# Kernel optimization log

Hardware: AMD Instinct MI355X
Metric: run time of the kernel (lower is better)

The kernel has to match this reference:

```python
import jax, jax.numpy as jnp
import numpy as np

B, S, D = 2, 2048, 1024
H = 16
HD = D // H  # 64


def setup_inputs() -> dict:
    key = jax.random.key(0)
    k1, k2, k3, k4, k5, k6 = jax.random.split(key, 6)
    hidden_states = jax.random.normal(k1, (B, S, D), dtype=jnp.float32)
    attention_mask = jax.random.randint(k2, (B, S), 0, 2, dtype=jnp.int32)
    scale = 1.0 / np.sqrt(D)
    Wq = jax.random.normal(k3, (D, D), dtype=jnp.float32) * scale
    bq = jax.random.normal(k4, (D,), dtype=jnp.float32) * 0.02
    Wk = jax.random.normal(k5, (D, D), dtype=jnp.float32) * scale
    bk = jax.random.normal(k6, (D,), dtype=jnp.float32) * 0.02
    return {"hidden_states": hidden_states, "attention_mask": attention_mask,
            "Wq": Wq, "bq": bq, "Wk": Wk, "bk": bk}


def _split_heads(x):
    # [B, S, D] -> [B, H, S, HD]
    b, s, _ = x.shape
    return x.reshape(b, s, H, HD).transpose(0, 2, 1, 3)


def reference(hidden_states, attention_mask, Wq, bq, Wk, bk):
    dh = jnp.sqrt(jnp.float32(HD))
    q = _split_heads(hidden_states @ Wq + bq)            # [B,H,S,HD]
    k = _split_heads(hidden_states @ Wk + bk)            # [B,H,S,HD]
    v = q + k                                            # value = Q + K
    k_t = -jax.nn.log_sigmoid(-k)                        # negate the logsigmoid(-K) transform
    scores = jnp.einsum('bhqd,bhkd->bhqk', q, k_t) / dh  # [B,H,S,S]
    # mask applied on the QUERY axis (dim 2), broadcast over key axis (faithful to source)
    mask = (attention_mask[:, None, :, None] == 0)       # [B,1,S,1]
    scores = jnp.where(mask, jnp.float32(-10000.0), scores)
    probs = jax.nn.softmax(scores, axis=-1)              # dropout: eval mode (identity)
    ctx = jnp.einsum('bhqk,bhkd->bhqd', probs, v)        # [B,H,S,HD]
    ctx = ctx.transpose(0, 2, 1, 3).reshape(B, S, D)
    return ctx
```

## Files before the change

kernel.cpp:

```cpp
#include <hip/hip_runtime.h>
#include <hip/hip_bf16.h>

#define B_ 2
#define S_ 2048
#define D_ 1024
#define H_ 16
#define HD_ 64

typedef __attribute__((ext_vector_type(8))) short short8;
typedef __attribute__((ext_vector_type(4))) short short4v;
typedef __attribute__((ext_vector_type(4))) float float4v;

typedef const __attribute__((address_space(1))) void* gas_ptr;
typedef __attribute__((address_space(3))) void* las_ptr;

static __device__ inline void gl_lds16(const void* g, void* l) {
  __builtin_amdgcn_global_load_lds((gas_ptr)g, (las_ptr)l, 16, 0, 0);
}

static __device__ inline float b2f(__hip_bfloat16 h) { return __bfloat162float(h); }

static __device__ inline short f2bs(float x) {
  __hip_bfloat16 h = __float2bfloat16(x);
  union { __hip_bfloat16 h; short s; } u; u.h = h; return u.s;
}
static __device__ inline float bs2f(short s) {
  union { short s; __hip_bfloat16 h; } u; u.s = s; return __bfloat162float(u.h);
}
static __device__ inline short4v pk4(float a, float b, float c, float d) {
  union { __hip_bfloat162 h[2]; short4v s; } u;
  u.h[0] = __float22bfloat162_rn(float2{a, b});
  u.h[1] = __float22bfloat162_rn(float2{c, d});
  return u.s;
}

static __device__ inline float4v mfma32(short8 a, short8 b, float4v c) {
  return __builtin_amdgcn_mfma_f32_16x16x32_bf16(a, b, c, 0, 0, 0);
}
static __device__ inline float4v mfma16(short4v a, short4v b, float4v c) {
  return __builtin_amdgcn_mfma_f32_16x16x16bf16_1k(a, b, c, 0, 0, 0);
}

__global__ __launch_bounds__(256) void pre(
    const float* __restrict__ Wq, const float* __restrict__ Wk,
    const float* __restrict__ hs,
    __hip_bfloat16* __restrict__ Wqt, __hip_bfloat16* __restrict__ Wkt,
    __hip_bfloat16* __restrict__ hsb) {
  if (blockIdx.z == 2) {
    const int blk = blockIdx.y * 16 + blockIdx.x;
    for (int it = 0; it < 8; ++it) {
      const size_t i = (size_t)blk * 16384 + it * 2048 + threadIdx.x * 8;
      const float4v v0 = *(const float4v*)(hs + i);
      const float4v v1 = *(const float4v*)(hs + i + 4);
      short8 s;
      for (int j = 0; j < 4; ++j) { s[j] = f2bs(v0[j]); s[4 + j] = f2bs(v1[j]); }
      *(short8*)(hsb + i) = s;
    }
    return;
  }
  const float* W = blockIdx.z ? Wk : Wq;
  __hip_bfloat16* Wt = blockIdx.z ? Wkt : Wqt;
  __shared__ float t[64][65];
  const int n0 = blockIdx.x * 64, k0 = blockIdx.y * 64;
  const int c = threadIdx.x & 63, r0 = threadIdx.x >> 6;
  for (int i = 0; i < 16; ++i) {
    const int r = i * 4 + r0;
    t[c][r] = W[(size_t)(k0 + r) * D_ + n0 + c];
  }
  __syncthreads();
  for (int i = 0; i < 16; ++i) {
    const int rr = i * 4 + r0;
    Wt[(size_t)(n0 + rr) * D_ + k0 + c] = __float2bfloat16(t[rr][c]);
  }
}

__global__ __launch_bounds__(256) void gemm_fused(
    const __hip_bfloat16* __restrict__ A,
    const __hip_bfloat16* __restrict__ Wqt, const __hip_bfloat16* __restrict__ Wkt,
    const float* __restrict__ bq, const float* __restrict__ bk,
    __hip_bfloat16* __restrict__ q_out, __hip_bfloat16* __restrict__ kt_out,
    __hip_bfloat16* __restrict__ vT) {
  const int n0 = blockIdx.x * 128, m0 = blockIdx.y * 64;
  __shared__ __hip_bfloat16 As[2][64 * 32];
  __shared__ __hip_bfloat16 Bq[2][128 * 32];
  __shared__ __hip_bfloat16 Bk[2][128 * 32];
  const int tid = threadIdx.x, wid = tid >> 6, lane = tid & 63;
  const int wm = (wid >> 1) * 32, wn = (wid & 1) * 64;
  const int l15 = lane & 15, l4 = lane >> 4;
  const float4v zz = {0.f, 0.f, 0.f, 0.f};
  float4v accq[2][4], acck[2][4];
  for (int i = 0; i < 2; ++i)
    for (int j = 0; j < 4; ++j) { accq[i][j] = zz; acck[i][j] = zz; }
  const int arow = wid * 16 + (lane >> 2);
  const int brow = wid * 32 + (lane >> 2);
  const int lk8 = (lane & 3) * 8;
  gl_lds16(A + (size_t)(m0 + arow) * D_ + lk8, As[0] + wid * 512);
  gl_lds16(Wqt + (size_t)(n0 + brow) * D_ + lk8, Bq[0] + wid * 1024);
  gl_lds16(Wqt + (size_t)(n0 + brow + 16) * D_ + lk8, Bq[0] + wid * 1024 + 512);
  gl_lds16(Wkt + (size_t)(n0 + brow) * D_ + lk8, Bk[0] + wid * 1024);
  gl_lds16(Wkt + (size_t)(n0 + brow + 16) * D_ + lk8, Bk[0] + wid * 1024 + 512);
  int p = 0;
  for (int kb = 0; kb < 32; ++kb) {
    __syncthreads();
    if (kb < 31) {
      const int kc = (kb + 1) * 32 + lk8;
      gl_lds16(A + (size_t)(m0 + arow) * D_ + kc, As[p ^ 1] + wid * 512);
      gl_lds16(Wqt + (size_t)(n0 + brow) * D_ + kc, Bq[p ^ 1] + wid * 1024);
      gl_lds16(Wqt + (size_t)(n0 + brow + 16) * D_ + kc, Bq[p ^ 1] + wid * 1024 + 512);
      gl_lds16(Wkt + (size_t)(n0 + brow) * D_ + kc, Bk[p ^ 1] + wid * 1024);
      gl_lds16(Wkt + (size_t)(n0 + brow + 16) * D_ + kc, Bk[p ^ 1] + wid * 1024 + 512);
    }
    short8 af[2], bfq[4], bfk[4];
    const int fo = l4 * 8;
    for (int rt = 0; rt < 2; ++rt)
      af[rt] = *(const short8*)(As[p] + (wm + rt * 16 + l15) * 32 + fo);
    for (int ct = 0; ct < 4; ++ct) {
      bfq[ct] = *(const short8*)(Bq[p] + (wn + ct * 16 + l15) * 32 + fo);
      bfk[ct] = *(const short8*)(Bk[p] + (wn + ct * 16 + l15) * 32 + fo);
    }
    for (int rt = 0; rt < 2; ++rt)
      for (int ct = 0; ct < 4; ++ct) {
        accq[rt][ct] = mfma32(af[rt], bfq[ct], accq[rt][ct]);
        acck[rt][ct] = mfma32(af[rt], bfk[ct], acck[rt][ct]);
      }
    p ^= 1;
  }
  float bvq[4], bvk[4];
  for (int ct = 0; ct < 4; ++ct) {
    bvq[ct] = bq[n0 + wn + ct * 16 + l15];
    bvk[ct] = bk[n0 + wn + ct * 16 + l15];
  }
  for (int rt = 0; rt < 2; ++rt)
    for (int ct = 0; ct < 4; ++ct) {
      const int col = n0 + wn + ct * 16 + l15;
      const int h = col >> 6, d = col & 63;
      const int rowb = m0 + wm + rt * 16 + l4 * 4;
      short4v vv;
      for (int r = 0; r < 4; ++r) {
        const int row = rowb + r;
        const float qv = accq[rt][ct][r] + bvq[ct];
        const float kv = acck[rt][ct][r] + bvk[ct];
        const float sp = fmaxf(kv, 0.f) + __logf(1.f + __expf(-fabsf(kv)));
        q_out[(size_t)row * D_ + col] = __float2bfloat16(qv);
        kt_out[(size_t)row * D_ + col] = __float2bfloat16(sp);
        vv[r] = f2bs(qv + kv);
      }
      const int b = rowb >> 11, s = rowb & 2047;
      *(short4v*)(vT + ((size_t)(b * H_ + h) * HD_ + d) * S_ + s) = vv;
    }
}

__global__ __launch_bounds__(256, 4) void attn(
    const __hip_bfloat16* __restrict__ qb, const __hip_bfloat16* __restrict__ ktb,
    const __hip_bfloat16* __restrict__ vT, const int* __restrict__ mask,
    float* __restrict__ out) {
  __shared__ short smem[17664];
  const int q0 = blockIdx.x * 128, h = blockIdx.y, b = blockIdx.z;
  const int tid = threadIdx.x, wid = tid >> 6, lane = tid & 63;
  const int l15 = lane & 15, l4 = lane >> 4;
  const __hip_bfloat16* qh = qb + (size_t)b * S_ * D_ + h * HD_;
  const __hip_bfloat16* kh = ktb + (size_t)b * S_ * D_ + h * HD_;
  const __hip_bfloat16* vh = vT + (size_t)(b * H_ + h) * HD_ * S_;
  const int srow = tid >> 2;
  const int b0 = tid & 3;
  const int sh = srow & 7;
  const int w0 = srow * 64 + ((b0 ^ sh) * 8);
  const int w1 = srow * 64 + (((b0 + 4) ^ sh) * 8);

  const int qlA = wid * 32 + l15, qlB = qlA + 16;
  const int qrA = q0 + qlA, qrB = q0 + qlB;
  const float SC = 0.125f * 1.44269504f;
  const float mqA = (mask[b * S_ + qrA] != 0) ? SC : 0.f;
  const float mqB = (mask[b * S_ + qrB] != 0) ? SC : 0.f;
  const short8 rA0 = *(const short8*)(qh + (size_t)qrA * D_ + l4 * 8);
  const short8 rA1 = *(const short8*)(qh + (size_t)qrA * D_ + 32 + l4 * 8);
  const short8 rB0 = *(const short8*)(qh + (size_t)qrB * D_ + l4 * 8);
  const short8 rB1 = *(const short8*)(qh + (size_t)qrB * D_ + 32 + l4 * 8);
  short8 bqA0, bqA1, bqB0, bqB1;
  for (int j = 0; j < 8; ++j) {
    bqA0[j] = f2bs(bs2f(rA0[j]) * mqA);
    bqA1[j] = f2bs(bs2f(rA1[j]) * mqA);
    bqB0[j] = f2bs(bs2f(rB0[j]) * mqB);
    bqB1[j] = f2bs(bs2f(rB1[j]) * mqB);
  }

  const int lsh = l15 & 7;
  const int ak0off = l15 * 64 + ((l4 ^ lsh) * 8);
  const int ak1off = l15 * 64 + (((l4 + 4) ^ lsh) * 8);
  int avoff[4];
#pragma unroll
  for (int t = 0; t < 4; ++t)
    avoff[t] = 4096 + l15 * 64 + (((2 * t + (l4 >> 1)) ^ lsh) * 8) + (l4 & 1) * 4;

  const float4v zz = {0.f, 0.f, 0.f, 0.f};
  float4v oaccA[4] = {zz, zz, zz, zz};
  float4v oaccB[4] = {zz, zz, zz, zz};
  float lsumA = 0.f, lsumB = 0.f;

  short8 gk0 = *(const short8*)(kh + (size_t)srow * D_ + b0 * 8);
  short8 gk1 = *(const short8*)(kh + (size_t)srow * D_ + b0 * 8 + 32);
  short8 gv0 = *(const short8*)(vh + (size_t)srow * S_ + b0 * 8);
  short8 gv1 = *(const short8*)(vh + (size_t)srow * S_ + b0 * 8 + 32);

  int p = 0;
  for (int c = 0; c < 32; ++c) {
    short* bufp = smem + p * 8192;
    *(short8*)(bufp + w0) = gk0;
    *(short8*)(bufp + w1) = gk1;
    *(short8*)(bufp + 4096 + w0) = gv0;
    *(short8*)(bufp + 4096 + w1) = gv1;
    __syncthreads();
    if (c < 31) {
      const int kb = (c + 1) * 64;
      gk0 = *(const short8*)(kh + (size_t)(kb + srow) * D_ + b0 * 8);
      gk1 = *(const short8*)(kh + (size_t)(kb + srow) * D_ + b0 * 8 + 32);
      gv0 = *(const short8*)(vh + (size_t)srow * S_ + kb + b0 * 8);
      gv1 = *(const short8*)(vh + (size_t)srow * S_ + kb + b0 * 8 + 32);
    }
#pragma unroll
    for (int t = 0; t < 4; ++t) {
      const short8 ak0 = *(const short8*)(bufp + t * 1024 + ak0off);
      const short8 ak1 = *(const short8*)(bufp + t * 1024 + ak1off);
      float4v cA = zz, cB = zz;
      cA = mfma32(ak0, bqA0, cA);
      cA = mfma32(ak1, bqA1, cA);
      cB = mfma32(ak0, bqB0, cB);
      cB = mfma32(ak1, bqB1, cB);
      float eA[4], eB[4];
#pragma unroll
      for (int r = 0; r < 4; ++r) {
        eA[r] = __builtin_amdgcn_exp2f(cA[r]); lsumA += eA[r];
        eB[r] = __builtin_amdgcn_exp2f(cB[r]); lsumB += eB[r];
      }
      const short4v pfA = pk4(eA[0], eA[1], eA[2], eA[3]);
      const short4v pfB = pk4(eB[0], eB[1], eB[2], eB[3]);
#pragma unroll
      for (int dt = 0; dt < 4; ++dt) {
        const short4v av = *(const short4v*)(bufp + dt * 1024 + avoff[t]);
        oaccA[dt] = mfma16(av, pfA, oaccA[dt]);
        oaccB[dt] = mfma16(av, pfB, oaccB[dt]);
      }
    }
    p ^= 1;
  }
  float lA = lsumA + __shfl_xor(lsumA, 16); lA += __shfl_xor(lA, 32);
  float lB = lsumB + __shfl_xor(lsumB, 16); lB += __shfl_xor(lB, 32);
  __syncthreads();
  float* mbuf = (float*)smem;
  float* mlb = (float*)smem + 128 * 68;
#pragma unroll
  for (int dt = 0; dt < 4; ++dt)
#pragma unroll
    for (int r = 0; r < 4; ++r) {
      mbuf[qlA * 68 + dt * 16 + l4 * 4 + r] = oaccA[dt][r];
      mbuf[qlB * 68 + dt * 16 + l4 * 4 + r] = oaccB[dt][r];
    }
  if (l4 == 0) { mlb[qlA] = lA; mlb[qlB] = lB; }
  __syncthreads();
  const int qq = tid >> 1;
  const int dg = (tid & 1) * 32;
  const float li = 1.f / mlb[qq];
  float* orow = out + (size_t)(b * S_ + q0 + qq) * D_ + h * HD_ + dg;
#pragma unroll
  for (int i = 0; i < 8; ++i) {
    float4v v = *(const float4v*)&mbuf[qq * 68 + dg + i * 4];
#pragma unroll
    for (int r = 0; r < 4; ++r) v[r] *= li;
    *(float4v*)(orow + i * 4) = v;
  }
}

extern "C" void kernel_launch(void* const* d_in, const int* in_sizes, int n_in,
                              void* d_out, int out_size, void* d_ws, size_t ws_size,
                              hipStream_t stream) {
  const float* hs = (const float*)d_in[0];
  const int* mask = (const int*)d_in[1];
  const float* Wq = (const float*)d_in[2];
  const float* bq = (const float*)d_in[3];
  const float* Wk = (const float*)d_in[4];
  const float* bk = (const float*)d_in[5];
  float* out = (float*)d_out;
  char* ws = (char*)d_ws;
  const size_t MB = 1u << 20;
  __hip_bfloat16* q_b = (__hip_bfloat16*)(ws + 0 * MB);
  __hip_bfloat16* k_b = (__hip_bfloat16*)(ws + 8 * MB);
  __hip_bfloat16* hsb = (__hip_bfloat16*)(ws + 16 * MB);
  __hip_bfloat16* vT  = (__hip_bfloat16*)(ws + 24 * MB);
  __hip_bfloat16* Wqt = (__hip_bfloat16*)(ws + 32 * MB);
  __hip_bfloat16* Wkt = (__hip_bfloat16*)(ws + 34 * MB);

  pre<<<dim3(16, 16, 3), 256, 0, stream>>>(Wq, Wk, hs, Wqt, Wkt, hsb);
  gemm_fused<<<dim3(8, 64), 256, 0, stream>>>(hsb, Wqt, Wkt, bq, bk, q_b, k_b, vT);
  attn<<<dim3(16, 16, 2), 256, 0, stream>>>(q_b, k_b, vT, mask, out);
}
```

Measured before the change: 181.3 us.

## Permute V^T sequence layout for wide LDS reads and remap attention blocks per XCD

The GEMM epilogue now writes V^T with a permuted sequence index inside each 64-key chunk. The attention kernel can then load its PV operands with two 16-byte LDS reads per 16-row tile instead of four 8-byte reads, and the PV MFMAs are regrouped after all four probability tiles are computed. The attention grid is flattened to 1D so that all 16 query blocks of one (batch, head) pair land on the same XCD, which should improve L2 reuse of K and V. The cost is more live registers for the buffered probability tiles.

```diff
diff --git a/kernel.cpp b/kernel.cpp
--- a/kernel.cpp
+++ b/kernel.cpp
@@ -146,7 +146,8 @@
         vv[r] = f2bs(qv + kv);
       }
       const int b = rowb >> 11, s = rowb & 2047;
-      *(short4v*)(vT + ((size_t)(b * H_ + h) * HD_ + d) * S_ + s) = vv;
+      const int sw = (s & ~63) | (((s >> 4) & 3) << 2) | (((s >> 2) & 3) << 4);
+      *(short4v*)(vT + ((size_t)(b * H_ + h) * HD_ + d) * S_ + sw) = vv;
     }
 }
 
@@ -155,7 +156,12 @@
     const __hip_bfloat16* __restrict__ vT, const int* __restrict__ mask,
     float* __restrict__ out) {
   __shared__ short smem[17664];
-  const int q0 = blockIdx.x * 128, h = blockIdx.y, b = blockIdx.z;
+  const int id = blockIdx.x;
+  const int xcd = id & 7;
+  const int rest = id >> 3;
+  const int q0 = (rest & 15) * 128;
+  const int hb = (rest >> 4) * 8 + xcd;
+  const int h = hb >> 1, b = hb & 1;
   const int tid = threadIdx.x, wid = tid >> 6, lane = tid & 63;
   const int l15 = lane & 15, l4 = lane >> 4;
   const __hip_bfloat16* qh = qb + (size_t)b * S_ * D_ + h * HD_;
@@ -187,10 +193,8 @@
   const int lsh = l15 & 7;
   const int ak0off = l15 * 64 + ((l4 ^ lsh) * 8);
   const int ak1off = l15 * 64 + (((l4 + 4) ^ lsh) * 8);
-  int avoff[4];
-#pragma unroll
-  for (int t = 0; t < 4; ++t)
-    avoff[t] = 4096 + l15 * 64 + (((2 * t + (l4 >> 1)) ^ lsh) * 8) + (l4 & 1) * 4;
+  const int vb0off = 4096 + ((2 * l4) ^ lsh) * 8;
+  const int vb1off = 4096 + ((2 * l4 + 1) ^ lsh) * 8;
 
   const float4v zz = {0.f, 0.f, 0.f, 0.f};
   float4v oaccA[4] = {zz, zz, zz, zz};
@@ -217,6 +221,7 @@
       gv0 = *(const short8*)(vh + (size_t)srow * S_ + kb + b0 * 8);
       gv1 = *(const short8*)(vh + (size_t)srow * S_ + kb + b0 * 8 + 32);
     }
+    short4v pA[4], pB[4];
 #pragma unroll
     for (int t = 0; t < 4; ++t) {
       const short8 ak0 = *(const short8*)(bufp + t * 1024 + ak0off);
@@ -232,14 +237,26 @@
         eA[r] = __builtin_amdgcn_exp2f(cA[r]); lsumA += eA[r];
         eB[r] = __builtin_amdgcn_exp2f(cB[r]); lsumB += eB[r];
       }
-      const short4v pfA = pk4(eA[0], eA[1], eA[2], eA[3]);
-      const short4v pfB = pk4(eB[0], eB[1], eB[2], eB[3]);
-#pragma unroll
-      for (int dt = 0; dt < 4; ++dt) {
-        const short4v av = *(const short4v*)(bufp + dt * 1024 + avoff[t]);
-        oaccA[dt] = mfma16(av, pfA, oaccA[dt]);
-        oaccB[dt] = mfma16(av, pfB, oaccB[dt]);
-      }
+      pA[t] = pk4(eA[0], eA[1], eA[2], eA[3]);
+      pB[t] = pk4(eB[0], eB[1], eB[2], eB[3]);
+    }
+#pragma unroll
+    for (int dt = 0; dt < 4; ++dt) {
+      const int rb = (dt * 16 + l15) * 64;
+      const short8 av0 = *(const short8*)(bufp + rb + vb0off);
+      const short8 av1 = *(const short8*)(bufp + rb + vb1off);
+      const short4v a0 = {av0[0], av0[1], av0[2], av0[3]};
+      const short4v a1 = {av0[4], av0[5], av0[6], av0[7]};
+      const short4v a2 = {av1[0], av1[1], av1[2], av1[3]};
+      const short4v a3 = {av1[4], av1[5], av1[6], av1[7]};
+      oaccA[dt] = mfma16(a0, pA[0], oaccA[dt]);
+      oaccB[dt] = mfma16(a0, pB[0], oaccB[dt]);
+      oaccA[dt] = mfma16(a1, pA[1], oaccA[dt]);
+      oaccB[dt] = mfma16(a1, pB[1], oaccB[dt]);
+      oaccA[dt] = mfma16(a2, pA[2], oaccA[dt]);
+      oaccB[dt] = mfma16(a2, pB[2], oaccB[dt]);
+      oaccA[dt] = mfma16(a3, pA[3], oaccA[dt]);
+      oaccB[dt] = mfma16(a3, pB[3], oaccB[dt]);
     }
     p ^= 1;
   }
@@ -291,5 +308,5 @@
 
   pre<<<dim3(16, 16, 3), 256, 0, stream>>>(Wq, Wk, hs, Wqt, Wkt, hsb);
   gemm_fused<<<dim3(8, 64), 256, 0, stream>>>(hsb, Wqt, Wkt, bq, bk, q_b, k_b, vT);
-  attn<<<dim3(16, 16, 2), 256, 0, stream>>>(q_b, k_b, vT, mask, out);
-}
+  attn<<<dim3(512), 256, 0, stream>>>(q_b, k_b, vT, mask, out);
+}
```

Measured after the change: 166.7 us. -8.1%, faster.
